# Optimization experiments

Measured on AMD Instinct MI355X. Metric: run time of the kernel, lower is better.

Reference implementation:

```python
import jax, jax.numpy as jnp
import numpy as np

B, T, D, H = 2, 2048, 2048, 16
HD = D // H  # head_dim = 128
NEG = -1e9


def setup_inputs() -> dict:
    key = jax.random.key(0)
    k1, k2, k3 = jax.random.split(key, 3)
    x = jax.random.normal(k1, (B, T, D), dtype=jnp.float32)
    # additive causal mask: 0 on/below diagonal, large negative above
    mask = jnp.where(jnp.tril(jnp.ones((T, T), dtype=bool)), 0.0, NEG).astype(jnp.float32)
    causal_mask = mask[None, None]  # [1,1,T,T]
    w_qkv = jax.random.normal(k2, (3 * D, D), dtype=jnp.float32) * (D ** -0.5)
    w_out = jax.random.normal(k3, (D, D), dtype=jnp.float32) * (D ** -0.5)
    b_out = jnp.zeros((D,), dtype=jnp.float32)
    return {"x": x, "causal_mask": causal_mask, "w_qkv": w_qkv, "w_out": w_out, "b_out": b_out}


def reference(x, causal_mask, w_qkv, w_out, b_out):
    scale = HD ** -0.5
    qkv = jnp.einsum('btd,ed->bte', x, w_qkv)          # [B,T,3D]
    q, k, v = jnp.split(qkv, 3, axis=-1)
    def heads(t):  # [B,T,D] -> [B,H,T,HD]
        return t.reshape(B, T, H, HD).transpose(0, 2, 1, 3)
    q, k, v = heads(q), heads(k), heads(v)
    attn = jnp.einsum('bhqd,bhkd->bhqk', q, k) * scale + causal_mask
    attn = jax.nn.softmax(attn, axis=-1)
    out = jnp.einsum('bhqk,bhkd->bhqd', attn, v)       # [B,H,T,HD]
    out = out.transpose(0, 2, 1, 3).reshape(B, T, D)
    return jnp.einsum('btd,ed->bte', out, w_out) + b_out
```

## Files before the change

### kernel.cpp

```cpp
#include <hip/hip_runtime.h>
#include <stdint.h>

typedef uint16_t u16;
typedef __attribute__((ext_vector_type(8))) short short8;
typedef __attribute__((ext_vector_type(4))) float f32x4;
typedef __attribute__((ext_vector_type(16))) float f32x16;

#define MFMA16(a, b, c) __builtin_amdgcn_mfma_f32_16x16x32_bf16((a), (b), (c), 0, 0, 0)
#define MFMA32(a, b, c) __builtin_amdgcn_mfma_f32_32x32x16_bf16((a), (b), (c), 0, 0, 0)
#define AS1 __attribute__((address_space(1)))
#define AS3 __attribute__((address_space(3)))

__device__ __forceinline__ void gld_lds16(const u16* g, u16* l) {
  __builtin_amdgcn_global_load_lds((const AS1 void*)g, (AS3 void*)l, 16, 0, 0);
}

__device__ __forceinline__ u16 f2bf(float f) {
  uint32_t u = __float_as_uint(f);
  u += 0x7fffu + ((u >> 16) & 1u);
  return (u16)(u >> 16);
}

__global__ __launch_bounds__(256) void cvt_all(const float* __restrict__ x,
                                               const float* __restrict__ wqkv,
                                               const float* __restrict__ wout,
                                               u16* __restrict__ xb,
                                               u16* __restrict__ wqkvb,
                                               u16* __restrict__ woutb) {
  const int n1 = 8388608 / 8, n2 = 12582912 / 8;
  int i = blockIdx.x * 256 + threadIdx.x;
  const float* src;
  u16* dst;
  int j;
  if (i < n1) {
    src = x; dst = xb; j = i;
  } else if (i < n1 + n2) {
    src = wqkv; dst = wqkvb; j = i - n1;
  } else {
    src = wout; dst = woutb; j = i - n1 - n2;
  }
  float4 v0 = ((const float4*)src)[j * 2];
  float4 v1 = ((const float4*)src)[j * 2 + 1];
  uint4 o;
  o.x = (uint32_t)f2bf(v0.x) | ((uint32_t)f2bf(v0.y) << 16);
  o.y = (uint32_t)f2bf(v0.z) | ((uint32_t)f2bf(v0.w) << 16);
  o.z = (uint32_t)f2bf(v1.x) | ((uint32_t)f2bf(v1.y) << 16);
  o.w = (uint32_t)f2bf(v1.z) | ((uint32_t)f2bf(v1.w) << 16);
  ((uint4*)dst)[j] = o;
}

template <int N>
__device__ __forceinline__ void bar_vm() {
  asm volatile("s_waitcnt vmcnt(%0)\n\ts_barrier" ::"n"(N) : "memory");
}
__device__ __forceinline__ void bar_fence() {
  asm volatile("s_barrier" ::: "memory");
}

__global__ __launch_bounds__(512, 2) void proj8_gemm(const u16* __restrict__ xb,
                                                     const u16* __restrict__ wqkvb,
                                                     u16* __restrict__ qkb) {
  constexpr int ASZ = 256 * 64;
  constexpr int NT = 32;
  __shared__ u16 sm[4 * ASZ];

  int bx = blockIdx.x;
  bx = (bx & 7) * 32 + (bx >> 3);
  const int mt = bx >> 4, nt = bx & 15;
  const u16* Ab = xb + (size_t)mt * 256 * 2048;
  const u16* Bb = wqkvb + (size_t)nt * 256 * 2048;
  u16* C = qkb + (size_t)mt * 256 * 4096 + nt * 256;

  const int tid = threadIdx.x, lane = tid & 63, w = tid >> 6;
  const int wm = w >> 2, wn = w & 3;
  const int lo = lane & 15, q4 = lane >> 4;

  f32x4 acc[8][4];
  const f32x4 fzero = {0.f, 0.f, 0.f, 0.f};
#pragma unroll
  for (int i = 0; i < 8; ++i)
#pragma unroll
    for (int j = 0; j < 4; ++j) acc[i][j] = fzero;

  auto stage_half = [&](int tau, int h) {
    const int slot = tau & 1;
    const int k0 = tau * 64;
    const u16* G = (h < 2) ? Bb : Ab;
    u16* L = sm + (h < 2 ? 2 * ASZ : 0) + slot * ASZ;
#pragma unroll
    for (int s = 0; s < 2; ++s) {
      const int c = tid + s * 512;
      const int hr = c >> 3, pc = c & 7;
      const int r = (h < 2) ? (h * 128 + hr)
                            : ((hr & 63) + ((hr >> 6) << 7) + ((h & 1) << 6));
      const int c4 = pc ^ (r & 7);
      gld_lds16(G + (size_t)r * 2048 + k0 + c4 * 8, L + r * 64 + pc * 8);
    }
  };

  stage_half(0, 0);
  stage_half(0, 1);
  stage_half(0, 2);
  stage_half(0, 3);
  bar_vm<2>();

  for (int tau = 0; tau < NT; ++tau) {
    const u16* As = sm + (tau & 1) * ASZ;
    const u16* Bs = sm + 2 * ASZ + (tau & 1) * ASZ;
    short8 bf[8];
#pragma unroll
    for (int q = 0; q < 4; ++q) {
      if (tau + 1 < NT) stage_half(tau + 1, q);
      if (q == 0) {
#pragma unroll
        for (int j = 0; j < 4; ++j)
#pragma unroll
          for (int kk = 0; kk < 2; ++kk) {
            const int r = wn * 64 + j * 16 + lo;
            bf[j * 2 + kk] =
                *(const short8*)(Bs + r * 64 + (((kk * 4 + q4) ^ (r & 7)) * 8));
          }
      }
      short8 af[2][2];
#pragma unroll
      for (int i = 0; i < 2; ++i)
#pragma unroll
        for (int kk = 0; kk < 2; ++kk) {
          const int r = wm * 128 + q * 32 + i * 16 + lo;
          af[i][kk] =
              *(const short8*)(As + r * 64 + (((kk * 4 + q4) ^ (r & 7)) * 8));
        }
      bar_fence();
      __builtin_amdgcn_s_setprio(1);
#pragma unroll
      for (int i = 0; i < 2; ++i)
#pragma unroll
        for (int j = 0; j < 4; ++j)
#pragma unroll
          for (int kk = 0; kk < 2; ++kk)
            acc[q * 2 + i][j] = MFMA16(af[i][kk], bf[j * 2 + kk], acc[q * 2 + i][j]);
      __builtin_amdgcn_s_setprio(0);
      if (q == 0) {
        if (tau == NT - 1) bar_vm<0>();
        else bar_vm<2>();
      } else if (q == 1) {
        bar_vm<4>();
      } else if (q == 2) {
        bar_vm<6>();
      } else {
        if (tau < NT - 1) bar_vm<2>();
      }
    }
  }

  const float sc =
      (nt < 8) ? (0.08838834764831843f * 1.4426950408889634f) : 1.0f;
#pragma unroll
  for (int i = 0; i < 8; ++i)
#pragma unroll
    for (int j = 0; j < 4; ++j) {
      const int col = wn * 64 + j * 16 + lo;
#pragma unroll
      for (int e = 0; e < 4; ++e) {
        const int row = wm * 128 + i * 16 + q4 * 4 + e;
        C[(size_t)row * 4096 + col] = f2bf(acc[i][j][e] * sc);
      }
    }
}

template <int MFR>
__device__ __forceinline__ void gemm_core3(const u16* __restrict__ Ab,
                                           const u16* __restrict__ Bb,
                                           u16* sm, int tid,
                                           f32x4 acc[MFR][4]) {
  constexpr int AROWS = MFR * 32;
  constexpr int ASZ = AROWS * 32;
  constexpr int BSZ = 128 * 32;
  constexpr int BUF = ASZ + BSZ;
  constexpr int NT = 64;
  constexpr int ALD = AROWS / 64;
  constexpr int VN = ALD + 2;

  const int lane = tid & 63, w = tid >> 6;
  const int wr = w >> 1, wc = w & 1;
  const int lo = lane & 15, q4 = lane >> 4;
  const int pcl = (((lo & 1) << 2) | q4) ^ ((lo >> 1) & 7);
  const int loff = (lo >> 1) * 64 + pcl * 8;

  auto stage = [&](int g) {
    u16* As = sm + (g % 3) * BUF;
    u16* Bs = As + ASZ;
    const int k0 = g * 32;
#pragma unroll
    for (int s = 0; s < ALD; ++s) {
      const int c = tid + s * 256;
      const int sr = c >> 3, pc = c & 7;
      const int t = pc ^ (sr & 7);
      const int r = sr * 2 + (t >> 2), c4 = t & 3;
      gld_lds16(Ab + (size_t)r * 2048 + k0 + c4 * 8, As + c * 8);
    }
#pragma unroll
    for (int s = 0; s < 2; ++s) {
      const int c = tid + s * 256;
      const int sr = c >> 3, pc = c & 7;
      const int t = pc ^ (sr & 7);
      const int r = sr * 2 + (t >> 2), c4 = t & 3;
      gld_lds16(Bb + (size_t)r * 2048 + k0 + c4 * 8, Bs + c * 8);
    }
  };

  stage(0);
  stage(1);
  bar_vm<VN>();

  for (int g = 0; g < NT; ++g) {
    const u16* As = sm + (g % 3) * BUF;
    const u16* Bs = As + ASZ;
    if (g + 2 < NT) stage(g + 2);
    short8 af[MFR], bf[4];
#pragma unroll
    for (int i = 0; i < MFR; ++i)
      af[i] = *(const short8*)(As + (wr * (MFR * 16) + i * 16) * 32 + loff);
#pragma unroll
    for (int j = 0; j < 4; ++j)
      bf[j] = *(const short8*)(Bs + (wc * 64 + j * 16) * 32 + loff);
    __builtin_amdgcn_s_setprio(1);
#pragma unroll
    for (int i = 0; i < MFR; ++i)
#pragma unroll
      for (int j = 0; j < 4; ++j) acc[i][j] = MFMA16(af[i], bf[j], acc[i][j]);
    __builtin_amdgcn_s_setprio(0);
    if (g + 1 < NT) {
      if (g + 2 < NT) {
        bar_vm<VN>();
      } else {
        bar_vm<0>();
      }
    }
  }
}

__global__ __launch_bounds__(256, 2) void vproj_gemm(const u16* __restrict__ wqkvb,
                                                     const u16* __restrict__ xb,
                                                     u16* __restrict__ vtb) {
  __shared__ u16 sm[3 * (128 * 32 + 128 * 32)];
  int bx = blockIdx.x;
  bx = (bx & 7) * 64 + (bx >> 3);
  const int tid = threadIdx.x;
  const int mt = bx >> 5, nt = bx & 31;
  const u16* Ab = wqkvb + (size_t)(4096 + mt * 128) * 2048;
  const u16* Bb = xb + (size_t)nt * 128 * 2048;
  u16* C = vtb + (size_t)mt * 128 * 4096 + nt * 128;
  f32x4 acc[4][4];
  const f32x4 fzero = {0.f, 0.f, 0.f, 0.f};
#pragma unroll
  for (int i = 0; i < 4; ++i)
#pragma unroll
    for (int j = 0; j < 4; ++j) acc[i][j] = fzero;

  gemm_core3<4>(Ab, Bb, sm, tid, acc);

  const int lane = tid & 63, w = tid >> 6;
  const int wr = w >> 1, wc = w & 1;
  const int lo = lane & 15, q4 = lane >> 4;
#pragma unroll
  for (int i = 0; i < 4; ++i)
#pragma unroll
    for (int j = 0; j < 4; ++j) {
      const int col = wc * 64 + j * 16 + lo;
#pragma unroll
      for (int e = 0; e < 4; ++e) {
        const int row = wr * 64 + i * 16 + q4 * 4 + e;
        C[(size_t)row * 4096 + col] = f2bf(acc[i][j][e]);
      }
    }
}

__global__ __launch_bounds__(256, 2) void out_gemm(const u16* __restrict__ A,
                                                   const u16* __restrict__ B,
                                                   float* __restrict__ Cf,
                                                   const float* __restrict__ bias) {
  __shared__ u16 sm[3 * (128 * 32 + 128 * 32)];
  int bx = blockIdx.x;
  bx = (bx & 7) * 64 + (bx >> 3);
  const int tid = threadIdx.x;
  const int mt = bx >> 4, nt = bx & 15;
  const u16* Ab = A + (size_t)mt * 128 * 2048;
  const u16* Bb = B + (size_t)nt * 128 * 2048;
  f32x4 acc[4][4];
  const f32x4 fzero = {0.f, 0.f, 0.f, 0.f};
#pragma unroll
  for (int i = 0; i < 4; ++i)
#pragma unroll
    for (int j = 0; j < 4; ++j) acc[i][j] = fzero;

  gemm_core3<4>(Ab, Bb, sm, tid, acc);

  const int lane = tid & 63, w = tid >> 6;
  const int wr = w >> 1, wc = w & 1;
  const int lo = lane & 15, q4 = lane >> 4;
#pragma unroll
  for (int i = 0; i < 4; ++i)
#pragma unroll
    for (int j = 0; j < 4; ++j) {
      const int col = nt * 128 + wc * 64 + j * 16 + lo;
      const float bv = bias[col];
#pragma unroll
      for (int e = 0; e < 4; ++e) {
        const int row = mt * 128 + wr * 64 + i * 16 + q4 * 4 + e;
        Cf[(size_t)row * 2048 + col] = acc[i][j][e] + bv;
      }
    }
}

__global__ __launch_bounds__(512) void flash_attn(const u16* __restrict__ qk,
                                                  const u16* __restrict__ vt,
                                                  u16* __restrict__ aout) {
  constexpr int T = 2048, WQK = 4096, D = 2048;
  constexpr int KT = 64 * 128;
  __shared__ u16 smem[4 * KT + 512];

  const int bx = blockIdx.x;
  const int g = bx & 31;
  const int h = g & 15, b = g >> 4;
  const int qt = (bx < 256) ? (bx >> 5) : (15 - ((bx - 256) >> 5));
  const int q0 = qt * 128;
  const int tid = threadIdx.x, lane = tid & 63, w = tid >> 6;
  const int wr = w & 3, wk = w >> 2;
  const int l31 = lane & 31, hi = lane >> 5;

  const u16* Qb = qk + (size_t)b * T * WQK + h * 128;
  const u16* Kb = Qb + 2048;
  const u16* Vtb = vt + (size_t)h * 128 * 4096 + b * 2048;
  float* fex = (float*)smem;

  short8 qf[8];
#pragma unroll
  for (int kc = 0; kc < 8; ++kc)
    qf[kc] = *(const short8*)(Qb + (size_t)(q0 + wr * 32 + l31) * WQK +
                              kc * 16 + hi * 8);

  f32x16 o[4];
  float osum = 0.f;
#pragma unroll
  for (int dt = 0; dt < 4; ++dt)
#pragma unroll
    for (int e = 0; e < 16; ++e) o[dt][e] = 0.f;

  auto stage = [&](int kt) {
    const int kv0 = kt * 64;
    u16* Kl = smem + (kt & 1) * KT;
    u16* Vl = smem + 2 * KT + (kt & 1) * KT;
#pragma unroll
    for (int s = 0; s < 2; ++s) {
      const int c = tid + s * 512;
      {
        const int r = c >> 4, pc = c & 15;
        const int gc = pc ^ (r & 7);
        gld_lds16(Kb + (size_t)(kv0 + r) * WQK + gc * 8, Kl + c * 8);
      }
      {
        const int r = c >> 3, pc = c & 7;
        const int gc = pc ^ (r & 7);
        gld_lds16(Vtb + (size_t)r * 4096 + kv0 + gc * 8, Vl + c * 8);
      }
    }
  };

  stage(0);
  const int ktmax = 2 * qt + 1;
  for (int kt = 0; kt <= ktmax; ++kt) {
    __syncthreads();
    if (kt < ktmax) stage(kt + 1);
    const u16* Ksc = smem + (kt & 1) * KT;
    const u16* Vsc = smem + 2 * KT + (kt & 1) * KT;

    f32x16 s2;
#pragma unroll
    for (int e = 0; e < 16; ++e) s2[e] = 0.f;
    const int rk = wk * 32 + l31;
    __builtin_amdgcn_s_setprio(1);
#pragma unroll
    for (int kc = 0; kc < 8; ++kc) {
      short8 kf =
          *(const short8*)&Ksc[rk * 128 + (((kc * 2 + hi) ^ (rk & 7)) * 8)];
      s2 = MFMA32(kf, qf[kc], s2);
    }
    __builtin_amdgcn_s_setprio(0);

    const bool diag = (kt >= 2 * qt);
#pragma unroll
    for (int r = 0; r < 16; ++r) {
      float e = exp2f(s2[r]);
      if (diag) {
        const int kcol = kt * 64 + wk * 32 + (r & 3) + 8 * (r >> 2) + 4 * hi;
        const int qrow = q0 + wr * 32 + l31;
        if (kcol > qrow) e = 0.f;
      }
      s2[r] = e;
      osum += e;
    }

    short8 pa2[2];
#pragma unroll
    for (int ks2 = 0; ks2 < 2; ++ks2) {
      uint32_t y0, y1, y2, y3;
      asm("v_cvt_pk_bf16_f32 %0, %1, %2"
          : "=v"(y0) : "v"(s2[ks2 * 8 + 0]), "v"(s2[ks2 * 8 + 1]));
      asm("v_cvt_pk_bf16_f32 %0, %1, %2"
          : "=v"(y1) : "v"(s2[ks2 * 8 + 2]), "v"(s2[ks2 * 8 + 3]));
      asm("v_cvt_pk_bf16_f32 %0, %1, %2"
          : "=v"(y2) : "v"(s2[ks2 * 8 + 4]), "v"(s2[ks2 * 8 + 5]));
      asm("v_cvt_pk_bf16_f32 %0, %1, %2"
          : "=v"(y3) : "v"(s2[ks2 * 8 + 6]), "v"(s2[ks2 * 8 + 7]));
      asm volatile("v_permlane32_swap_b32 %0, %1" : "+v"(y0), "+v"(y2));
      asm volatile("v_permlane32_swap_b32 %0, %1" : "+v"(y1), "+v"(y3));
      int4 t4;
      t4.x = (int)y0; t4.y = (int)y1; t4.z = (int)y2; t4.w = (int)y3;
      pa2[ks2] = *(short8*)&t4;
    }

    __builtin_amdgcn_s_setprio(1);
#pragma unroll
    for (int ks2 = 0; ks2 < 2; ++ks2) {
#pragma unroll
      for (int dt = 0; dt < 4; ++dt) {
        const int rv = dt * 32 + l31;
        short8 vf = *(const short8*)&Vsc[rv * 64 +
                                         (((wk * 4 + ks2 * 2 + hi) ^ (rv & 7)) * 8)];
        o[dt] = MFMA32(pa2[ks2], vf, o[dt]);
      }
    }
    __builtin_amdgcn_s_setprio(0);
  }

  const float osum_full = osum + __shfl_xor(osum, 32);
  __syncthreads();
  if (wk == 1) {
#pragma unroll
    for (int dt = 0; dt < 4; ++dt)
#pragma unroll
      for (int r = 0; r < 16; ++r) {
        const int qr = wr * 32 + (r & 3) + 8 * (r >> 2) + 4 * hi;
        fex[qr * 128 + dt * 32 + l31] = o[dt][r];
      }
  }
  if (hi == 0) fex[16384 + wk * 128 + wr * 32 + l31] = osum_full;
  __syncthreads();
  if (wk == 0) {
#pragma unroll
    for (int r = 0; r < 16; ++r) {
      const int qr = wr * 32 + (r & 3) + 8 * (r >> 2) + 4 * hi;
      const float st = fex[16384 + qr] + fex[16384 + 128 + qr];
      const float inv = 1.f / st;
#pragma unroll
      for (int dt = 0; dt < 4; ++dt) {
        const float v = o[dt][r] + fex[qr * 128 + dt * 32 + l31];
        aout[(size_t)(b * T + q0 + qr) * D + h * 128 + dt * 32 + l31] =
            f2bf(v * inv);
      }
    }
  }
}

extern "C" void kernel_launch(void* const* d_in, const int* in_sizes, int n_in,
                              void* d_out, int out_size, void* d_ws, size_t ws_size,
                              hipStream_t stream) {
  const float* x = (const float*)d_in[0];
  const float* w_qkv = (const float*)d_in[2];
  const float* w_out = (const float*)d_in[3];
  const float* b_out = (const float*)d_in[4];
  float* out = (float*)d_out;

  const int BT = 4096, D = 2048, D3 = 6144;
  u16* xb = (u16*)d_ws;
  u16* wqkvb = xb + (size_t)BT * D;
  u16* woutb = wqkvb + (size_t)D3 * D;
  u16* qkb = woutb + (size_t)D * D;
  u16* vtb = qkb + (size_t)BT * 4096;
  u16* attnb = vtb + (size_t)D * BT;

  const int total8 = (BT * D + D3 * D + D * D) / 8;
  cvt_all<<<total8 / 256, 256, 0, stream>>>(x, w_qkv, w_out, xb, wqkvb, woutb);
  proj8_gemm<<<256, 512, 0, stream>>>(xb, wqkvb, qkb);
  vproj_gemm<<<512, 256, 0, stream>>>(wqkvb, xb, vtb);
  flash_attn<<<512, 512, 0, stream>>>(qkb, vtb, attnb);
  out_gemm<<<512, 256, 0, stream>>>(attnb, woutb, out, b_out);
}
```

Baseline: 345.5 us.

## Restructure GEMM staging to prefetch two k-tiles ahead with fewer barriers

Changes the QKV projection GEMM main loop from four per-quarter staging steps and four barriers per k-tile to a scheme that loads the B half of the next tile and the A half two tiles ahead. It now runs one barrier after the first quarter and one vmcnt wait at the end of each iteration. The aim is to cut synchronisation overhead and deepen the global-to-LDS prefetch so load latency is hidden behind MFMAs. It relies on the double-buffered LDS slots being safe to overwrite at the new points, which adds a risk of races if the slot ordering is wrong.

```diff
diff --git a/kernel.cpp b/kernel.cpp
--- a/kernel.cpp
+++ b/kernel.cpp
@@ -102,25 +102,56 @@
   stage_half(0, 1);
   stage_half(0, 2);
   stage_half(0, 3);
-  bar_vm<2>();
+  stage_half(1, 0);
+  stage_half(1, 1);
+  bar_vm<0>();
 
   for (int tau = 0; tau < NT; ++tau) {
     const u16* As = sm + (tau & 1) * ASZ;
     const u16* Bs = sm + 2 * ASZ + (tau & 1) * ASZ;
+
+    if (tau + 1 < NT) {
+      stage_half(tau + 1, 2);
+      stage_half(tau + 1, 3);
+    }
     short8 bf[8];
 #pragma unroll
-    for (int q = 0; q < 4; ++q) {
-      if (tau + 1 < NT) stage_half(tau + 1, q);
-      if (q == 0) {
+    for (int j = 0; j < 4; ++j)
+#pragma unroll
+      for (int kk = 0; kk < 2; ++kk) {
+        const int r = wn * 64 + j * 16 + lo;
+        bf[j * 2 + kk] =
+            *(const short8*)(Bs + r * 64 + (((kk * 4 + q4) ^ (r & 7)) * 8));
+      }
+    {
+      short8 af[2][2];
+#pragma unroll
+      for (int i = 0; i < 2; ++i)
+#pragma unroll
+        for (int kk = 0; kk < 2; ++kk) {
+          const int r = wm * 128 + 0 * 32 + i * 16 + lo;
+          af[i][kk] =
+              *(const short8*)(As + r * 64 + (((kk * 4 + q4) ^ (r & 7)) * 8));
+        }
+      __builtin_amdgcn_s_setprio(1);
+#pragma unroll
+      for (int i = 0; i < 2; ++i)
 #pragma unroll
         for (int j = 0; j < 4; ++j)
 #pragma unroll
-          for (int kk = 0; kk < 2; ++kk) {
-            const int r = wn * 64 + j * 16 + lo;
-            bf[j * 2 + kk] =
-                *(const short8*)(Bs + r * 64 + (((kk * 4 + q4) ^ (r & 7)) * 8));
-          }
-      }
+          for (int kk = 0; kk < 2; ++kk)
+            acc[i][j] = MFMA16(af[i][kk], bf[j * 2 + kk], acc[i][j]);
+      __builtin_amdgcn_s_setprio(0);
+    }
+    __builtin_amdgcn_sched_barrier(0);
+    bar_fence();
+
+    if (tau + 2 < NT) {
+      stage_half(tau + 2, 0);
+      stage_half(tau + 2, 1);
+    }
+#pragma unroll
+    for (int q = 1; q < 4; ++q) {
       short8 af[2][2];
 #pragma unroll
       for (int i = 0; i < 2; ++i)
@@ -130,7 +161,6 @@
           af[i][kk] =
               *(const short8*)(As + r * 64 + (((kk * 4 + q4) ^ (r & 7)) * 8));
         }
-      bar_fence();
       __builtin_amdgcn_s_setprio(1);
 #pragma unroll
       for (int i = 0; i < 2; ++i)
@@ -140,16 +170,12 @@
           for (int kk = 0; kk < 2; ++kk)
             acc[q * 2 + i][j] = MFMA16(af[i][kk], bf[j * 2 + kk], acc[q * 2 + i][j]);
       __builtin_amdgcn_s_setprio(0);
-      if (q == 0) {
-        if (tau == NT - 1) bar_vm<0>();
-        else bar_vm<2>();
-      } else if (q == 1) {
-        bar_vm<4>();
-      } else if (q == 2) {
-        bar_vm<6>();
-      } else {
-        if (tau < NT - 1) bar_vm<2>();
-      }
+    }
+
+    if (tau + 2 < NT) {
+      bar_vm<4>();
+    } else if (tau + 1 < NT) {
+      bar_vm<0>();
     }
   }
 
```

After: 340.1 us. No clear change (-1.6%).

## Deepen QKV GEMM prefetch pipeline by unrolling two k-tiles per iteration

Applied to the files above, without the earlier changes.

Restructures the projection GEMM main loop to process two k-tiles per iteration with a deeper prefetch. Up to seven quarter-tiles of global-to-LDS loads stay in flight instead of two, with the vmcnt waits retuned to match. It also adds an explicit lgkmcnt(0) wait and a sched_barrier before the MFMA block. This is meant to hide more global-load latency behind the MFMAs. The risk is that the hand-tuned wait counts cause stalls or races, and the per-phase barriers add synchronisation.

```diff
diff --git a/kernel.cpp b/kernel.cpp
--- a/kernel.cpp
+++ b/kernel.cpp
@@ -53,15 +53,11 @@
 __device__ __forceinline__ void bar_vm() {
   asm volatile("s_waitcnt vmcnt(%0)\n\ts_barrier" ::"n"(N) : "memory");
 }
-__device__ __forceinline__ void bar_fence() {
-  asm volatile("s_barrier" ::: "memory");
-}
 
 __global__ __launch_bounds__(512, 2) void proj8_gemm(const u16* __restrict__ xb,
                                                      const u16* __restrict__ wqkvb,
                                                      u16* __restrict__ qkb) {
   constexpr int ASZ = 256 * 64;
-  constexpr int NT = 32;
   __shared__ u16 sm[4 * ASZ];
 
   int bx = blockIdx.x;
@@ -102,53 +98,73 @@
   stage_half(0, 1);
   stage_half(0, 2);
   stage_half(0, 3);
-  bar_vm<2>();
-
-  for (int tau = 0; tau < NT; ++tau) {
-    const u16* As = sm + (tau & 1) * ASZ;
-    const u16* Bs = sm + 2 * ASZ + (tau & 1) * ASZ;
-    short8 bf[8];
-#pragma unroll
-    for (int q = 0; q < 4; ++q) {
-      if (tau + 1 < NT) stage_half(tau + 1, q);
-      if (q == 0) {
-#pragma unroll
-        for (int j = 0; j < 4; ++j)
+  stage_half(1, 0);
+  stage_half(1, 1);
+  stage_half(1, 2);
+  bar_vm<8>();
+
+  for (int j = 0; j < 16; ++j) {
+    const bool full = (j < 15);
+#pragma unroll
+    for (int t = 0; t < 2; ++t) {
+      const u16* As = sm + t * ASZ;
+      const u16* Bs = sm + 2 * ASZ + t * ASZ;
+      short8 bf[8];
+#pragma unroll
+      for (int q = 0; q < 4; ++q) {
+        const int ph = t * 4 + q;
+        if (ph == 0) {
+          stage_half(2 * j + 1, 3);
+        } else if (full) {
+          if (ph <= 4) stage_half(2 * j + 2, ph - 1);
+          else stage_half(2 * j + 3, ph - 5);
+        }
+        if (q == 0) {
+#pragma unroll
+          for (int jj = 0; jj < 4; ++jj)
+#pragma unroll
+            for (int kk = 0; kk < 2; ++kk) {
+              const int r = wn * 64 + jj * 16 + lo;
+              bf[jj * 2 + kk] =
+                  *(const short8*)(Bs + r * 64 + (((kk * 4 + q4) ^ (r & 7)) * 8));
+            }
+        }
+        short8 af[2][2];
+#pragma unroll
+        for (int i = 0; i < 2; ++i)
 #pragma unroll
           for (int kk = 0; kk < 2; ++kk) {
-            const int r = wn * 64 + j * 16 + lo;
-            bf[j * 2 + kk] =
-                *(const short8*)(Bs + r * 64 + (((kk * 4 + q4) ^ (r & 7)) * 8));
+            const int r = wm * 128 + q * 32 + i * 16 + lo;
+            af[i][kk] =
+                *(const short8*)(As + r * 64 + (((kk * 4 + q4) ^ (r & 7)) * 8));
           }
-      }
-      short8 af[2][2];
-#pragma unroll
-      for (int i = 0; i < 2; ++i)
-#pragma unroll
-        for (int kk = 0; kk < 2; ++kk) {
-          const int r = wm * 128 + q * 32 + i * 16 + lo;
-          af[i][kk] =
-              *(const short8*)(As + r * 64 + (((kk * 4 + q4) ^ (r & 7)) * 8));
+        __builtin_amdgcn_s_barrier();
+        asm volatile("s_waitcnt lgkmcnt(0)" ::: "memory");
+        __builtin_amdgcn_sched_barrier(0);
+        __builtin_amdgcn_s_setprio(1);
+#pragma unroll
+        for (int i = 0; i < 2; ++i)
+#pragma unroll
+          for (int jj = 0; jj < 4; ++jj)
+#pragma unroll
+            for (int kk = 0; kk < 2; ++kk)
+              acc[q * 2 + i][jj] =
+                  MFMA16(af[i][kk], bf[jj * 2 + kk], acc[q * 2 + i][jj]);
+        __builtin_amdgcn_s_setprio(0);
+        if (ph == 1) {
+          if (full) bar_vm<10>();
+          else bar_vm<8>();
+        } else if (ph == 3) {
+          if (full) bar_vm<8>();
+          else bar_vm<2>();
+        } else if (ph == 5) {
+          if (full) bar_vm<10>();
+          else bar_vm<0>();
+        } else if (ph == 7) {
+          if (full) bar_vm<8>();
+        } else {
+          __builtin_amdgcn_s_barrier();
         }
-      bar_fence();
-      __builtin_amdgcn_s_setprio(1);
-#pragma unroll
-      for (int i = 0; i < 2; ++i)
-#pragma unroll
-        for (int j = 0; j < 4; ++j)
-#pragma unroll
-          for (int kk = 0; kk < 2; ++kk)
-            acc[q * 2 + i][j] = MFMA16(af[i][kk], bf[j * 2 + kk], acc[q * 2 + i][j]);
-      __builtin_amdgcn_s_setprio(0);
-      if (q == 0) {
-        if (tau == NT - 1) bar_vm<0>();
-        else bar_vm<2>();
-      } else if (q == 1) {
-        bar_vm<4>();
-      } else if (q == 2) {
-        bar_vm<6>();
-      } else {
-        if (tau < NT - 1) bar_vm<2>();
       }
     }
   }
```

New measurement: 351.2 us. No clear change (+1.7%).
